# Optimization experiments

Measured on AMD Instinct MI355X. Metric: run time of the kernel, lower is better.

## Reference

```python
import jax, jax.numpy as jnp
import numpy as np

HIDDEN = 1024
D_FF = 2816
N_EXPERTS = 8
TOP_K = 2
TEMPERATURE = 1.0
LB_WEIGHT = 0.01


def setup_inputs() -> dict:
    key = jax.random.key(0)
    ks = jax.random.split(key, 5)
    scale_h = 1.0 / np.sqrt(HIDDEN)
    scale_f = 1.0 / np.sqrt(D_FF)
    x = jax.random.normal(ks[0], (2, 1024, HIDDEN), dtype=jnp.float32)
    gate_w = jax.random.normal(ks[1], (N_EXPERTS, HIDDEN), dtype=jnp.float32) * scale_h
    w1 = jax.random.normal(ks[2], (N_EXPERTS, HIDDEN, D_FF), dtype=jnp.float32) * scale_h  # gate proj
    w3 = jax.random.normal(ks[3], (N_EXPERTS, HIDDEN, D_FF), dtype=jnp.float32) * scale_h  # up proj
    w2 = jax.random.normal(ks[4], (N_EXPERTS, D_FF, HIDDEN), dtype=jnp.float32) * scale_f  # down proj
    return {"x": x, "gate_w": gate_w, "w1": w1, "w3": w3, "w2": w2}


def reference(x, gate_w, w1, w3, w2):
    B, S, H = x.shape
    xf = x.reshape(-1, H)                       # [T, H]
    T = xf.shape[0]

    # gating (eval mode: no routing noise)
    gate_logits = xf @ gate_w.T                 # [T, E]
    scaled = gate_logits / TEMPERATURE
    topk_vals, topk_idx = jax.lax.top_k(scaled, TOP_K)   # [T, K]
    topk_probs = jax.nn.softmax(topk_vals, axis=-1)      # [T, K]

    # dense combine weights: weight of expert e for token t (0 if not selected)
    onehot = jax.nn.one_hot(topk_idx, N_EXPERTS, dtype=xf.dtype)  # [T, K, E]
    comb = jnp.einsum("tke,tk->te", onehot, topk_probs)           # [T, E]

    # per-expert SwiGLU on all tokens, masked combine (math equals gather/scatter)
    h1 = jnp.einsum("th,ehf->etf", xf, w1)      # [E, T, F]
    h3 = jnp.einsum("th,ehf->etf", xf, w3)
    act = jax.nn.silu(h1) * h3                  # [E, T, F]
    y = jnp.einsum("etf,efh->eth", act, w2)     # [E, T, H]
    out = jnp.einsum("te,eth->th", comb, y)     # [T, H]

    # auxiliary load-balancing loss
    gate_probs = jax.nn.softmax(gate_logits, axis=-1)             # [T, E]
    expert_usage = onehot.sum(axis=(0, 1)) / (T * TOP_K + 1e-9)   # [E]
    gate_importance = gate_probs.mean(axis=0)                     # [E]
    aux = jnp.sum(expert_usage * gate_importance) * N_EXPERTS
    aux_loss = jnp.minimum(aux * LB_WEIGHT, 1.0)

    return out.reshape(B, S, H), aux_loss
```

## Files before the change

kernel.cpp:

```cpp
#include <hip/hip_runtime.h>
#include <hip/hip_bf16.h>
#include <math.h>


#define T_TOK 2048
#define HID   1024
#define DFF   2816
#define NE    8
#define ROWS  4096

typedef unsigned short u16;
typedef __attribute__((ext_vector_type(8))) short bf16x8;
typedef __attribute__((ext_vector_type(4))) float f32x4;

#define OFF_CNT    0
#define OFF_IMP    64
#define OFF_OFFS   128
#define OFF_TOPKI  256
#define OFF_TOPKP  (OFF_TOPKI + 16384)
#define OFF_BTOK   (OFF_TOPKP + 16384)
#define OFF_BPRB   (OFF_BTOK + 65536)
#define OFF_XB     (OFF_BPRB + 65536)
#define OFF_W1T    (OFF_XB + 4194304)
#define OFF_W3T    (OFF_W1T + 46137344)
#define OFF_W2T    (OFF_W3T + 46137344)
#define OFF_ACT    (OFF_W2T + 46137344)
#define WS_NEEDED  (OFF_ACT + 23068672)

__device__ __forceinline__ u16 f2bf(float f) {
    unsigned u = __float_as_uint(f);
    u = (u + 0x7fffu + ((u >> 16) & 1u)) >> 16;
    return (u16)u;
}

__device__ __forceinline__ void glds16(const void* g, void* l) {
    __builtin_amdgcn_global_load_lds(
        (const __attribute__((address_space(1))) unsigned int*)g,
        (__attribute__((address_space(3))) unsigned int*)l, 16, 0, 0);
}

__global__ void cvt_x_kernel(const float* __restrict__ x, u16* __restrict__ xb) {
    int i = blockIdx.x * 256 + threadIdx.x;
    float4 v = ((const float4*)x)[i];
    union { u16 s[4]; unsigned long long q; } o;
    o.s[0] = f2bf(v.x); o.s[1] = f2bf(v.y); o.s[2] = f2bf(v.z); o.s[3] = f2bf(v.w);
    ((unsigned long long*)xb)[i] = o.q;
}

__global__ void transpose_kernel(const float* __restrict__ in, u16* __restrict__ out,
                                 int K, int N) {
    __shared__ float tile[64][65];
    const float* ip = in + (size_t)blockIdx.z * K * N;
    u16* op = out + (size_t)blockIdx.z * K * N;
    int n0 = blockIdx.x * 64, k0 = blockIdx.y * 64;
    int tid = threadIdx.x;
#pragma unroll
    for (int p = 0; p < 4; ++p) {
        int row = p * 16 + (tid >> 4);
        int v = (tid & 15) * 4;
        float4 d = *(const float4*)(ip + (size_t)(k0 + row) * N + n0 + v);
        tile[row][v] = d.x; tile[row][v + 1] = d.y; tile[row][v + 2] = d.z; tile[row][v + 3] = d.w;
    }
    __syncthreads();
#pragma unroll
    for (int p = 0; p < 2; ++p) {
        int n = p * 32 + (tid >> 3);
        int g = (tid & 7) * 8;
        u16 o[8];
#pragma unroll
        for (int j = 0; j < 8; ++j) o[j] = f2bf(tile[g + j][n]);
        *(bf16x8*)(op + (size_t)(n0 + n) * K + k0 + g) = *(bf16x8*)o;
    }
}

__global__ void gating_kernel(const float* __restrict__ x, const float* __restrict__ gw,
                              int* __restrict__ topki, float* __restrict__ topkp,
                              float* __restrict__ imp) {
    __shared__ float s_imp[NE];
    int tid = threadIdx.x;
    if (tid < NE) s_imp[tid] = 0.f;
    __syncthreads();
    int lane = tid & 63;
    int t = blockIdx.x * 8 + (tid >> 6);
    float a[NE];
#pragma unroll
    for (int e = 0; e < NE; ++e) a[e] = 0.f;
#pragma unroll
    for (int c = 0; c < 16; ++c) {
        float xv = x[(size_t)t * HID + c * 64 + lane];
#pragma unroll
        for (int e = 0; e < NE; ++e) a[e] += xv * gw[e * HID + c * 64 + lane];
    }
#pragma unroll
    for (int e = 0; e < NE; ++e) {
#pragma unroll
        for (int off = 32; off > 0; off >>= 1) a[e] += __shfl_xor(a[e], off, 64);
    }
    if (lane == 0) {
        float v0 = -1e30f, v1 = -1e30f; int e0 = 0, e1 = 0;
#pragma unroll
        for (int e = 0; e < NE; ++e) {
            if (a[e] > v0) { v1 = v0; e1 = e0; v0 = a[e]; e0 = e; }
            else if (a[e] > v1) { v1 = a[e]; e1 = e; }
        }
        float p0 = 1.f / (1.f + expf(v1 - v0));
        topki[2 * t] = e0; topki[2 * t + 1] = e1;
        topkp[2 * t] = p0; topkp[2 * t + 1] = 1.f - p0;
        float s = 0.f, pe[NE];
#pragma unroll
        for (int e = 0; e < NE; ++e) { pe[e] = expf(a[e] - v0); s += pe[e]; }
        float inv = 1.f / s;
#pragma unroll
        for (int e = 0; e < NE; ++e) atomicAdd(&s_imp[e], pe[e] * inv);
    }
    __syncthreads();
    if (tid < NE) atomicAdd(&imp[tid], s_imp[tid]);
}

__global__ void compact_kernel(const int* __restrict__ topki, const float* __restrict__ topkp,
                               int* __restrict__ cnt, int* __restrict__ btok,
                               float* __restrict__ bprb) {
    int idx = blockIdx.x * 256 + threadIdx.x;
    int e = topki[idx];
    int pos = atomicAdd(&cnt[e], 1);
    btok[e * T_TOK + pos] = idx >> 1;
    bprb[e * T_TOK + pos] = topkp[idx];
}

__global__ void finalize_kernel(const int* __restrict__ cnt, const float* __restrict__ imp,
                                int* __restrict__ offs, float* __restrict__ aux_out) {
    if (threadIdx.x == 0) {
        int off = 0; float s = 0.f;
        for (int e = 0; e < NE; ++e) {
            offs[e] = off; off += cnt[e];
            s += ((float)cnt[e] / (4096.f + 1e-9f)) * (imp[e] / 2048.f);
        }
        aux_out[0] = fminf(s * 8.f * 0.01f, 1.f);
    }
}

__global__ __launch_bounds__(256, 2)
void gemm1_kernel(const u16* __restrict__ xb, const u16* __restrict__ w1t,
                  const u16* __restrict__ w3t, u16* __restrict__ act,
                  const int* __restrict__ btok, const int* __restrict__ cnt,
                  const int* __restrict__ offs) {
    int e = blockIdx.z;
    int n_e = cnt[e];
    int m0 = blockIdx.y * 128;
    if (m0 >= n_e) return;
    int nn0 = blockIdx.x * 128;
    int base = offs[e];

    __shared__ __align__(16) u16 As[128 * 32];
    __shared__ __align__(16) u16 B1s[128 * 32];
    __shared__ __align__(16) u16 B3s[128 * 32];

    int tid = threadIdx.x, lane = tid & 63, wv = tid >> 6;
    int wm = (wv >> 1) * 64, wn = (wv & 1) * 64;
    int l15 = lane & 15, quad = lane >> 4;

    int row0 = tid >> 2, row1 = 64 + row0;
    int sub = (tid & 3) * 8;
    int t0 = (m0 + row0 < n_e) ? btok[e * T_TOK + m0 + row0] : 0;
    int t1 = (m0 + row1 < n_e) ? btok[e * T_TOK + m0 + row1] : 0;
    const u16* ga0 = xb + (size_t)t0 * HID + sub;
    const u16* ga1 = xb + (size_t)t1 * HID + sub;
    const u16* g10 = w1t + ((size_t)e * DFF + nn0 + row0) * HID + sub;
    const u16* g11 = w1t + ((size_t)e * DFF + nn0 + row1) * HID + sub;
    const u16* g30 = w3t + ((size_t)e * DFF + nn0 + row0) * HID + sub;
    const u16* g31 = w3t + ((size_t)e * DFF + nn0 + row1) * HID + sub;
    u16* la0 = As  + (size_t)(wv * 64) * 8;
    u16* la1 = As  + (size_t)(256 + wv * 64) * 8;
    u16* l10 = B1s + (size_t)(wv * 64) * 8;
    u16* l11 = B1s + (size_t)(256 + wv * 64) * 8;
    u16* l30 = B3s + (size_t)(wv * 64) * 8;
    u16* l31 = B3s + (size_t)(256 + wv * 64) * 8;

    f32x4 acc1[4][4] = {}, acc3[4][4] = {};

    for (int k0 = 0; k0 < HID; k0 += 32) {
        glds16(ga0 + k0, la0); glds16(ga1 + k0, la1);
        glds16(g10 + k0, l10); glds16(g11 + k0, l11);
        glds16(g30 + k0, l30); glds16(g31 + k0, l31);
        __syncthreads();
        bf16x8 af[4];
#pragma unroll
        for (int i = 0; i < 4; ++i)
            af[i] = *(const bf16x8*)&As[(wm + i * 16 + l15) * 32 + quad * 8];
#pragma unroll
        for (int j = 0; j < 4; ++j) {
            bf16x8 b1 = *(const bf16x8*)&B1s[(wn + j * 16 + l15) * 32 + quad * 8];
            bf16x8 b3 = *(const bf16x8*)&B3s[(wn + j * 16 + l15) * 32 + quad * 8];
#pragma unroll
            for (int i = 0; i < 4; ++i) {
                acc1[i][j] = __builtin_amdgcn_mfma_f32_16x16x32_bf16(af[i], b1, acc1[i][j], 0, 0, 0);
                acc3[i][j] = __builtin_amdgcn_mfma_f32_16x16x32_bf16(af[i], b3, acc3[i][j], 0, 0, 0);
            }
        }
        __syncthreads();
    }
#pragma unroll
    for (int i = 0; i < 4; ++i) {
#pragma unroll
        for (int r = 0; r < 4; ++r) {
            int m = m0 + wm + i * 16 + quad * 4 + r;
            if (m < n_e) {
#pragma unroll
                for (int j = 0; j < 4; ++j) {
                    float h1 = acc1[i][j][r], h3 = acc3[i][j][r];
                    float v = h1 / (1.f + expf(-h1)) * h3;
                    act[(size_t)(base + m) * DFF + nn0 + wn + j * 16 + l15] = f2bf(v);
                }
            }
        }
    }
}

__global__ __launch_bounds__(256, 2)
void gemm2_kernel(const u16* __restrict__ act, const u16* __restrict__ w2t,
                  float* __restrict__ out, const int* __restrict__ btok,
                  const float* __restrict__ bprb, const int* __restrict__ cnt,
                  const int* __restrict__ offs) {
    int e = blockIdx.z;
    int n_e = cnt[e];
    int m0 = blockIdx.y * 128;
    if (m0 >= n_e) return;
    int nn0 = blockIdx.x * 128;
    int base = offs[e];

    __shared__ __align__(16) u16 As[128 * 32];
    __shared__ __align__(16) u16 Bs[128 * 32];

    int tid = threadIdx.x, lane = tid & 63, wv = tid >> 6;
    int wm = (wv >> 1) * 64, wn = (wv & 1) * 64;
    int l15 = lane & 15, quad = lane >> 4;

    int row0 = tid >> 2, row1 = 64 + row0;
    int sub = (tid & 3) * 8;
    int r0c = (m0 + row0 < n_e) ? (base + m0 + row0) : base;
    int r1c = (m0 + row1 < n_e) ? (base + m0 + row1) : base;
    const u16* ga0 = act + (size_t)r0c * DFF + sub;
    const u16* ga1 = act + (size_t)r1c * DFF + sub;
    const u16* gb0 = w2t + ((size_t)e * HID + nn0 + row0) * DFF + sub;
    const u16* gb1 = w2t + ((size_t)e * HID + nn0 + row1) * DFF + sub;
    u16* la0 = As + (size_t)(wv * 64) * 8;
    u16* la1 = As + (size_t)(256 + wv * 64) * 8;
    u16* lb0 = Bs + (size_t)(wv * 64) * 8;
    u16* lb1 = Bs + (size_t)(256 + wv * 64) * 8;

    f32x4 acc[4][4] = {};

    for (int k0 = 0; k0 < DFF; k0 += 32) {
        glds16(ga0 + k0, la0); glds16(ga1 + k0, la1);
        glds16(gb0 + k0, lb0); glds16(gb1 + k0, lb1);
        __syncthreads();
        bf16x8 af[4];
#pragma unroll
        for (int i = 0; i < 4; ++i)
            af[i] = *(const bf16x8*)&As[(wm + i * 16 + l15) * 32 + quad * 8];
#pragma unroll
        for (int j = 0; j < 4; ++j) {
            bf16x8 bf = *(const bf16x8*)&Bs[(wn + j * 16 + l15) * 32 + quad * 8];
#pragma unroll
            for (int i = 0; i < 4; ++i)
                acc[i][j] = __builtin_amdgcn_mfma_f32_16x16x32_bf16(af[i], bf, acc[i][j], 0, 0, 0);
        }
        __syncthreads();
    }
#pragma unroll
    for (int i = 0; i < 4; ++i) {
#pragma unroll
        for (int r = 0; r < 4; ++r) {
            int m = m0 + wm + i * 16 + quad * 4 + r;
            if (m < n_e) {
                int t = btok[e * T_TOK + m];
                float p = bprb[e * T_TOK + m];
#pragma unroll
                for (int j = 0; j < 4; ++j)
                    atomicAdd(&out[(size_t)t * HID + nn0 + wn + j * 16 + l15], p * acc[i][j][r]);
            }
        }
    }
}

extern "C" void kernel_launch(void* const* d_in, const int* in_sizes, int n_in,
                              void* d_out, int out_size, void* d_ws, size_t ws_size,
                              hipStream_t stream) {
    if (ws_size < (size_t)WS_NEEDED) return;

    const float* x  = (const float*)d_in[0];
    const float* gw = (const float*)d_in[1];
    const float* w1 = (const float*)d_in[2];
    const float* w3 = (const float*)d_in[3];
    const float* w2 = (const float*)d_in[4];
    float* out = (float*)d_out;

    char* ws = (char*)d_ws;
    int*   cnt   = (int*)(ws + OFF_CNT);
    float* imp   = (float*)(ws + OFF_IMP);
    int*   offs  = (int*)(ws + OFF_OFFS);
    int*   topki = (int*)(ws + OFF_TOPKI);
    float* topkp = (float*)(ws + OFF_TOPKP);
    int*   btok  = (int*)(ws + OFF_BTOK);
    float* bprb  = (float*)(ws + OFF_BPRB);
    u16*   xb    = (u16*)(ws + OFF_XB);
    u16*   w1t   = (u16*)(ws + OFF_W1T);
    u16*   w3t   = (u16*)(ws + OFF_W3T);
    u16*   w2t   = (u16*)(ws + OFF_W2T);
    u16*   actb  = (u16*)(ws + OFF_ACT);

    hipMemsetAsync(ws, 0, 256, stream);
    hipMemsetAsync(d_out, 0, (size_t)out_size * sizeof(float), stream);

    cvt_x_kernel<<<2048, 256, 0, stream>>>(x, xb);
    transpose_kernel<<<dim3(DFF / 64, HID / 64, NE), 256, 0, stream>>>(w1, w1t, HID, DFF);
    transpose_kernel<<<dim3(DFF / 64, HID / 64, NE), 256, 0, stream>>>(w3, w3t, HID, DFF);
    transpose_kernel<<<dim3(HID / 64, DFF / 64, NE), 256, 0, stream>>>(w2, w2t, DFF, HID);

    gating_kernel<<<T_TOK / 8, 512, 0, stream>>>(x, gw, topki, topkp, imp);
    compact_kernel<<<ROWS / 256, 256, 0, stream>>>(topki, topkp, cnt, btok, bprb);
    finalize_kernel<<<1, 64, 0, stream>>>(cnt, imp, offs, out + (size_t)T_TOK * HID);

    gemm1_kernel<<<dim3(DFF / 128, T_TOK / 128, NE), 256, 0, stream>>>(
        xb, w1t, w3t, actb, btok, cnt, offs);
    gemm2_kernel<<<dim3(HID / 128, T_TOK / 128, NE), 256, 0, stream>>>(
        actb, w2t, out, btok, bprb, cnt, offs);
}
```

Before: 527.5 us.

## Swizzle LDS tiles, shrink gemm2 M-tile, replace atomic scatter with combine kernel

Applies an XOR swizzle to the LDS layout of both GEMMs to cut bank conflicts on MFMA operand reads. gemm2 now uses 64-row M tiles with higher occupancy and writes per-expert outputs to a float scratch buffer that reuses the w1t region, instead of atomically adding into the output. A new combine kernel gathers each token's two expert rows and takes the weighted sum, which also removes the output memset. The cost is an extra launch and a scratch round trip, and the scratch aliases w1t, which is safe only because gemm1 has already finished with it.

New measurement: 519.7 us. Within noise of the previous version (-1.5%).

```diff
diff --git a/kernel.cpp b/kernel.cpp
--- a/kernel.cpp
+++ b/kernel.cpp
@@ -19,8 +19,8 @@
 #define OFF_TOPKI  256
 #define OFF_TOPKP  (OFF_TOPKI + 16384)
 #define OFF_BTOK   (OFF_TOPKP + 16384)
-#define OFF_BPRB   (OFF_BTOK + 65536)
-#define OFF_XB     (OFF_BPRB + 65536)
+#define OFF_EPOS   (OFF_BTOK + 65536)
+#define OFF_XB     (OFF_EPOS + 65536)
 #define OFF_W1T    (OFF_XB + 4194304)
 #define OFF_W3T    (OFF_W1T + 46137344)
 #define OFF_W2T    (OFF_W3T + 46137344)
@@ -117,14 +117,14 @@
     if (tid < NE) atomicAdd(&imp[tid], s_imp[tid]);
 }
 
-__global__ void compact_kernel(const int* __restrict__ topki, const float* __restrict__ topkp,
+__global__ void compact_kernel(const int* __restrict__ topki,
                                int* __restrict__ cnt, int* __restrict__ btok,
-                               float* __restrict__ bprb) {
+                               int* __restrict__ epos) {
     int idx = blockIdx.x * 256 + threadIdx.x;
     int e = topki[idx];
     int pos = atomicAdd(&cnt[e], 1);
     btok[e * T_TOK + pos] = idx >> 1;
-    bprb[e * T_TOK + pos] = topkp[idx];
+    epos[idx] = (e << 11) | pos;
 }
 
 __global__ void finalize_kernel(const int* __restrict__ cnt, const float* __restrict__ imp,
@@ -160,7 +160,8 @@
     int l15 = lane & 15, quad = lane >> 4;
 
     int row0 = tid >> 2, row1 = 64 + row0;
-    int sub = (tid & 3) * 8;
+    int q = (tid & 3) ^ ((tid >> 3) & 3);
+    int sub = q * 8;
     int t0 = (m0 + row0 < n_e) ? btok[e * T_TOK + m0 + row0] : 0;
     int t1 = (m0 + row1 < n_e) ? btok[e * T_TOK + m0 + row1] : 0;
     const u16* ga0 = xb + (size_t)t0 * HID + sub;
@@ -169,12 +170,12 @@
     const u16* g11 = w1t + ((size_t)e * DFF + nn0 + row1) * HID + sub;
     const u16* g30 = w3t + ((size_t)e * DFF + nn0 + row0) * HID + sub;
     const u16* g31 = w3t + ((size_t)e * DFF + nn0 + row1) * HID + sub;
-    u16* la0 = As  + (size_t)(wv * 64) * 8;
-    u16* la1 = As  + (size_t)(256 + wv * 64) * 8;
-    u16* l10 = B1s + (size_t)(wv * 64) * 8;
-    u16* l11 = B1s + (size_t)(256 + wv * 64) * 8;
-    u16* l30 = B3s + (size_t)(wv * 64) * 8;
-    u16* l31 = B3s + (size_t)(256 + wv * 64) * 8;
+    u16* la0 = As  + (wv * 64) * 8;
+    u16* la1 = As  + (256 + wv * 64) * 8;
+    u16* l10 = B1s + (wv * 64) * 8;
+    u16* l11 = B1s + (256 + wv * 64) * 8;
+    u16* l30 = B3s + (wv * 64) * 8;
+    u16* l31 = B3s + (256 + wv * 64) * 8;
 
     f32x4 acc1[4][4] = {}, acc3[4][4] = {};
 
@@ -185,12 +186,16 @@
         __syncthreads();
         bf16x8 af[4];
 #pragma unroll
-        for (int i = 0; i < 4; ++i)
-            af[i] = *(const bf16x8*)&As[(wm + i * 16 + l15) * 32 + quad * 8];
+        for (int i = 0; i < 4; ++i) {
+            int R = wm + i * 16 + l15;
+            af[i] = *(const bf16x8*)&As[R * 32 + (quad ^ ((R >> 1) & 3)) * 8];
+        }
 #pragma unroll
         for (int j = 0; j < 4; ++j) {
-            bf16x8 b1 = *(const bf16x8*)&B1s[(wn + j * 16 + l15) * 32 + quad * 8];
-            bf16x8 b3 = *(const bf16x8*)&B3s[(wn + j * 16 + l15) * 32 + quad * 8];
+            int R = wn + j * 16 + l15;
+            int so = R * 32 + (quad ^ ((R >> 1) & 3)) * 8;
+            bf16x8 b1 = *(const bf16x8*)&B1s[so];
+            bf16x8 b3 = *(const bf16x8*)&B3s[so];
 #pragma unroll
             for (int i = 0; i < 4; ++i) {
                 acc1[i][j] = __builtin_amdgcn_mfma_f32_16x16x32_bf16(af[i], b1, acc1[i][j], 0, 0, 0);
@@ -216,51 +221,51 @@
     }
 }
 
-__global__ __launch_bounds__(256, 2)
+__global__ __launch_bounds__(256, 4)
 void gemm2_kernel(const u16* __restrict__ act, const u16* __restrict__ w2t,
-                  float* __restrict__ out, const int* __restrict__ btok,
-                  const float* __restrict__ bprb, const int* __restrict__ cnt,
+                  float* __restrict__ ybuf, const int* __restrict__ cnt,
                   const int* __restrict__ offs) {
     int e = blockIdx.z;
     int n_e = cnt[e];
-    int m0 = blockIdx.y * 128;
+    int m0 = blockIdx.y * 64;
     if (m0 >= n_e) return;
     int nn0 = blockIdx.x * 128;
     int base = offs[e];
 
-    __shared__ __align__(16) u16 As[128 * 32];
+    __shared__ __align__(16) u16 As[64 * 32];
     __shared__ __align__(16) u16 Bs[128 * 32];
 
     int tid = threadIdx.x, lane = tid & 63, wv = tid >> 6;
-    int wm = (wv >> 1) * 64, wn = (wv & 1) * 64;
+    int wn = wv * 32;
     int l15 = lane & 15, quad = lane >> 4;
 
-    int row0 = tid >> 2, row1 = 64 + row0;
-    int sub = (tid & 3) * 8;
-    int r0c = (m0 + row0 < n_e) ? (base + m0 + row0) : base;
-    int r1c = (m0 + row1 < n_e) ? (base + m0 + row1) : base;
-    const u16* ga0 = act + (size_t)r0c * DFF + sub;
-    const u16* ga1 = act + (size_t)r1c * DFF + sub;
+    int row0 = tid >> 2;
+    int q = (tid & 3) ^ ((tid >> 3) & 3);
+    int sub = q * 8;
+    int ra = (m0 + row0 < n_e) ? (base + m0 + row0) : base;
+    const u16* ga0 = act + (size_t)ra * DFF + sub;
     const u16* gb0 = w2t + ((size_t)e * HID + nn0 + row0) * DFF + sub;
-    const u16* gb1 = w2t + ((size_t)e * HID + nn0 + row1) * DFF + sub;
-    u16* la0 = As + (size_t)(wv * 64) * 8;
-    u16* la1 = As + (size_t)(256 + wv * 64) * 8;
-    u16* lb0 = Bs + (size_t)(wv * 64) * 8;
-    u16* lb1 = Bs + (size_t)(256 + wv * 64) * 8;
-
-    f32x4 acc[4][4] = {};
+    const u16* gb1 = w2t + ((size_t)e * HID + nn0 + 64 + row0) * DFF + sub;
+    u16* la0 = As + (wv * 64) * 8;
+    u16* lb0 = Bs + (wv * 64) * 8;
+    u16* lb1 = Bs + (256 + wv * 64) * 8;
+
+    f32x4 acc[4][2] = {};
 
     for (int k0 = 0; k0 < DFF; k0 += 32) {
-        glds16(ga0 + k0, la0); glds16(ga1 + k0, la1);
+        glds16(ga0 + k0, la0);
         glds16(gb0 + k0, lb0); glds16(gb1 + k0, lb1);
         __syncthreads();
         bf16x8 af[4];
 #pragma unroll
-        for (int i = 0; i < 4; ++i)
-            af[i] = *(const bf16x8*)&As[(wm + i * 16 + l15) * 32 + quad * 8];
-#pragma unroll
-        for (int j = 0; j < 4; ++j) {
-            bf16x8 bf = *(const bf16x8*)&Bs[(wn + j * 16 + l15) * 32 + quad * 8];
+        for (int i = 0; i < 4; ++i) {
+            int R = i * 16 + l15;
+            af[i] = *(const bf16x8*)&As[R * 32 + (quad ^ ((R >> 1) & 3)) * 8];
+        }
+#pragma unroll
+        for (int j = 0; j < 2; ++j) {
+            int R = wn + j * 16 + l15;
+            bf16x8 bf = *(const bf16x8*)&Bs[R * 32 + (quad ^ ((R >> 1) & 3)) * 8];
 #pragma unroll
             for (int i = 0; i < 4; ++i)
                 acc[i][j] = __builtin_amdgcn_mfma_f32_16x16x32_bf16(af[i], bf, acc[i][j], 0, 0, 0);
@@ -271,16 +276,31 @@
     for (int i = 0; i < 4; ++i) {
 #pragma unroll
         for (int r = 0; r < 4; ++r) {
-            int m = m0 + wm + i * 16 + quad * 4 + r;
+            int m = m0 + i * 16 + quad * 4 + r;
             if (m < n_e) {
-                int t = btok[e * T_TOK + m];
-                float p = bprb[e * T_TOK + m];
-#pragma unroll
-                for (int j = 0; j < 4; ++j)
-                    atomicAdd(&out[(size_t)t * HID + nn0 + wn + j * 16 + l15], p * acc[i][j][r]);
+#pragma unroll
+                for (int j = 0; j < 2; ++j)
+                    ybuf[(size_t)(base + m) * HID + nn0 + wn + j * 16 + l15] = acc[i][j][r];
             }
         }
     }
+}
+
+__global__ void combine_kernel(const float* __restrict__ ybuf, const int* __restrict__ epos,
+                               const float* __restrict__ topkp, const int* __restrict__ offs,
+                               float* __restrict__ out) {
+    int t = blockIdx.x;
+    int c = threadIdx.x * 4;
+    int ep0 = epos[2 * t], ep1 = epos[2 * t + 1];
+    int r0 = offs[ep0 >> 11] + (ep0 & 2047);
+    int r1 = offs[ep1 >> 11] + (ep1 & 2047);
+    float p0 = topkp[2 * t], p1 = topkp[2 * t + 1];
+    float4 a = *(const float4*)&ybuf[(size_t)r0 * HID + c];
+    float4 b = *(const float4*)&ybuf[(size_t)r1 * HID + c];
+    float4 o;
+    o.x = p0 * a.x + p1 * b.x; o.y = p0 * a.y + p1 * b.y;
+    o.z = p0 * a.z + p1 * b.z; o.w = p0 * a.w + p1 * b.w;
+    *(float4*)&out[(size_t)t * HID + c] = o;
 }
 
 extern "C" void kernel_launch(void* const* d_in, const int* in_sizes, int n_in,
@@ -302,15 +322,15 @@
     int*   topki = (int*)(ws + OFF_TOPKI);
     float* topkp = (float*)(ws + OFF_TOPKP);
     int*   btok  = (int*)(ws + OFF_BTOK);
-    float* bprb  = (float*)(ws + OFF_BPRB);
+    int*   epos  = (int*)(ws + OFF_EPOS);
     u16*   xb    = (u16*)(ws + OFF_XB);
     u16*   w1t   = (u16*)(ws + OFF_W1T);
     u16*   w3t   = (u16*)(ws + OFF_W3T);
     u16*   w2t   = (u16*)(ws + OFF_W2T);
     u16*   actb  = (u16*)(ws + OFF_ACT);
+    float* ybuf  = (float*)(ws + OFF_W1T);
 
     hipMemsetAsync(ws, 0, 256, stream);
-    hipMemsetAsync(d_out, 0, (size_t)out_size * sizeof(float), stream);
 
     cvt_x_kernel<<<2048, 256, 0, stream>>>(x, xb);
     transpose_kernel<<<dim3(DFF / 64, HID / 64, NE), 256, 0, stream>>>(w1, w1t, HID, DFF);
@@ -318,11 +338,12 @@
     transpose_kernel<<<dim3(HID / 64, DFF / 64, NE), 256, 0, stream>>>(w2, w2t, DFF, HID);
 
     gating_kernel<<<T_TOK / 8, 512, 0, stream>>>(x, gw, topki, topkp, imp);
-    compact_kernel<<<ROWS / 256, 256, 0, stream>>>(topki, topkp, cnt, btok, bprb);
+    compact_kernel<<<ROWS / 256, 256, 0, stream>>>(topki, cnt, btok, epos);
     finalize_kernel<<<1, 64, 0, stream>>>(cnt, imp, offs, out + (size_t)T_TOK * HID);
 
     gemm1_kernel<<<dim3(DFF / 128, T_TOK / 128, NE), 256, 0, stream>>>(
         xb, w1t, w3t, actb, btok, cnt, offs);
-    gemm2_kernel<<<dim3(HID / 128, T_TOK / 128, NE), 256, 0, stream>>>(
-        actb, w2t, out, btok, bprb, cnt, offs);
-}
+    gemm2_kernel<<<dim3(HID / 128, T_TOK / 64, NE), 256, 0, stream>>>(
+        actb, w2t, ybuf, cnt, offs);
+    combine_kernel<<<T_TOK, 256, 0, stream>>>(ybuf, epos, topkp, offs, out);
+}
```
